# Kernel tuning notes

Measured on AMD Instinct MI355X. Metric: run time of the kernel, lower is better.

## Reference

```python
import jax, jax.numpy as jnp
import numpy as np

NEG_SLOPE = 0.2  # PyG GATConv default leaky_relu slope
N_NODES, N_EDGES, F_IN, HID = 25000, 200000, 64, 128


def gat_layer(x, src, dst, W, a_src, a_dst, b, heads, ch):
    """PyG-style GATConv (concat=True, eval mode). x:[N,Fin] -> [N,heads*ch]."""
    N = x.shape[0]
    h = (x @ W).reshape(N, heads, ch)                      # [N,H,C]
    al_s = jnp.sum(h * a_src, axis=-1)                     # [N,H]
    al_d = jnp.sum(h * a_dst, axis=-1)                     # [N,H]
    e = jax.nn.leaky_relu(al_s[src] + al_d[dst], NEG_SLOPE)  # [E,H]
    # segment softmax over incoming edges of each dst node (stable)
    e = e - jax.ops.segment_max(e, dst, num_segments=N)[dst]
    ex = jnp.exp(e)
    alpha = ex / jax.ops.segment_sum(ex, dst, num_segments=N)[dst]  # [E,H]
    out = jax.ops.segment_sum(h[src] * alpha[:, :, None], dst, num_segments=N)  # [N,H,C]
    return out.reshape(N, heads * ch) + b


def setup_inputs() -> dict:
    key = jax.random.key(0)
    ks = jax.random.split(key, 24)
    def g(k, shape, fan_in):
        return jax.random.normal(k, shape, dtype=jnp.float32) / np.sqrt(fan_in)
    inp = {
        "x": jax.random.normal(ks[0], (N_NODES, F_IN), dtype=jnp.float32),
        "edge_index": jax.random.randint(ks[1], (2, N_EDGES), 0, N_NODES, dtype=jnp.int64) if jax.config.jax_enable_x64 else jax.random.randint(ks[1], (2, N_EDGES), 0, N_NODES).astype(jnp.int32),
        "liquor_idx": jax.random.randint(ks[2], (4096,), 0, N_NODES),
        "ingredient_idx": jax.random.randint(ks[3], (4096,), 0, N_NODES),
        "W1": g(ks[4], (F_IN, 8 * HID), F_IN), "a_s1": g(ks[5], (8, HID), HID), "a_d1": g(ks[6], (8, HID), HID), "b1": jnp.zeros((8 * HID,), jnp.float32),
        "W2": g(ks[7], (8 * HID, 8 * HID), 8 * HID), "a_s2": g(ks[8], (8, HID), HID), "a_d2": g(ks[9], (8, HID), HID), "b2": jnp.zeros((8 * HID,), jnp.float32),
        "W3": g(ks[10], (8 * HID, HID), 8 * HID), "a_s3": g(ks[11], (1, HID), HID), "a_d3": g(ks[12], (1, HID), HID), "b3": jnp.zeros((HID,), jnp.float32),
        # MLP scorer: 256 -> 128 -> 64 -> 1
        "mw1": g(ks[13], (2 * HID, HID), 2 * HID), "mb1": jnp.zeros((HID,), jnp.float32),
        "mw2": g(ks[14], (HID, HID // 2), HID), "mb2": jnp.zeros((HID // 2,), jnp.float32),
        "mw3": g(ks[15], (HID // 2, 1), HID // 2), "mb3": jnp.zeros((1,), jnp.float32),
    }
    return inp


def reference(x, edge_index, liquor_idx, ingredient_idx,
              W1, a_s1, a_d1, b1, W2, a_s2, a_d2, b2, W3, a_s3, a_d3, b3,
              mw1, mb1, mw2, mb2, mw3, mb3):
    N = x.shape[0]
    loops = jnp.arange(N, dtype=edge_index.dtype)  # GATConv adds self-loops
    src = jnp.concatenate([edge_index[0], loops])
    dst = jnp.concatenate([edge_index[1], loops])
    h = jax.nn.relu(gat_layer(x, src, dst, W1, a_s1, a_d1, b1, 8, HID))
    h = jax.nn.relu(gat_layer(h, src, dst, W2, a_s2, a_d2, b2, 8, HID))
    h = gat_layer(h, src, dst, W3, a_s3, a_d3, b3, 1, HID)
    pair = jnp.concatenate([h[liquor_idx], h[ingredient_idx]], axis=-1)  # [B,256]
    z = jax.nn.relu(pair @ mw1 + mb1)
    z = jax.nn.relu(z @ mw2 + mb2)
    z = z @ mw3 + mb3
    return jax.nn.sigmoid(z).squeeze(-1)
```

## Files before the change

kernel.cpp:

```cpp
#include <hip/hip_runtime.h>
#include <math.h>

#define NEG_SLOPE 0.2f

typedef short short8 __attribute__((ext_vector_type(8)));
typedef float f32x4 __attribute__((ext_vector_type(4)));

__device__ __forceinline__ float lrelu(float x){ return x > 0.f ? x : NEG_SLOPE * x; }

__device__ __forceinline__ unsigned short f2bf(float f){
  union { float f; unsigned u; } v; v.f = f;
  unsigned r = v.u + 0x7fff + ((v.u >> 16) & 1);
  return (unsigned short)(r >> 16);
}
__device__ __forceinline__ float bf2f(unsigned short u){
  union { unsigned u; float f; } v; v.u = ((unsigned)u) << 16; return v.f;
}

__device__ __forceinline__ void gld16(const unsigned short* g, unsigned short* l){
  __builtin_amdgcn_global_load_lds(
      (const __attribute__((address_space(1))) unsigned int*)g,
      (__attribute__((address_space(3))) unsigned int*)l, 16, 0, 0);
}

#define MFMA_BF16 __builtin_amdgcn_mfma_f32_16x16x32_bf16

__global__ void k_count(const int* __restrict__ dst, int* __restrict__ cnt, int E){
  int e = blockIdx.x*blockDim.x + threadIdx.x;
  if (e < E) atomicAdd(&cnt[dst[e]], 1);
}

__global__ void k_blockscan(const int* __restrict__ cnt, int* __restrict__ row,
                            int* __restrict__ aux, int n){
  __shared__ int buf[256];
  int t = threadIdx.x;
  int base = blockIdx.x * 256;
  int v = (base + t < n) ? cnt[base + t] : 0;
  buf[t] = v;
  __syncthreads();
  #pragma unroll
  for (int off = 1; off < 256; off <<= 1){
    int u = (t >= off) ? buf[t - off] : 0;
    __syncthreads();
    buf[t] += u;
    __syncthreads();
  }
  if (base + t < n) row[base + t + 1] = buf[t];
  if (t == 255) aux[blockIdx.x] = buf[255];
  if (blockIdx.x == 0 && t == 0) row[0] = 0;
}

__global__ void k_addoff(const int* __restrict__ aux, int* __restrict__ row, int n){
  __shared__ int sbuf[256];
  int b = blockIdx.x, t = threadIdx.x;
  sbuf[t] = (t < b) ? aux[t] : 0;
  __syncthreads();
  #pragma unroll
  for (int off = 128; off >= 1; off >>= 1){
    if (t < off) sbuf[t] += sbuf[t + off];
    __syncthreads();
  }
  int i = b * 256 + t;
  if (i < n) row[i + 1] += sbuf[0];
}

__global__ void k_scatter(const int* __restrict__ src, const int* __restrict__ dst,
                          const int* __restrict__ row, int* __restrict__ cur,
                          int* __restrict__ csr, int E){
  int e = blockIdx.x*blockDim.x + threadIdx.x;
  if (e < E){
    int d = dst[e];
    int p = atomicAdd(&cur[d], 1);
    csr[row[d] + p] = src[e];
  }
}

__global__ void k_prep(const float* __restrict__ x, unsigned short* __restrict__ xb, int nx, int nxb,
                       const float* __restrict__ W1, unsigned short* __restrict__ Wt1,
                       const float* __restrict__ W2, unsigned short* __restrict__ Wt2,
                       const float* __restrict__ W3, unsigned short* __restrict__ Wt3,
                       const float* __restrict__ a_s1, const float* __restrict__ a_d1,
                       float* __restrict__ ws1){
  __shared__ float tile[32][33];
  int b = blockIdx.x, t = threadIdx.x;
  if (b < nxb){
    int i0 = b * 2048 + t * 8;
    if (i0 + 8 <= nx){
      float4 f0 = *reinterpret_cast<const float4*>(x + i0);
      float4 f1 = *reinterpret_cast<const float4*>(x + i0 + 4);
      short8 o;
      o[0]=f2bf(f0.x); o[1]=f2bf(f0.y); o[2]=f2bf(f0.z); o[3]=f2bf(f0.w);
      o[4]=f2bf(f1.x); o[5]=f2bf(f1.y); o[6]=f2bf(f1.z); o[7]=f2bf(f1.w);
      *reinterpret_cast<short8*>(xb + i0) = o;
    } else {
      for (int k = 0; k < 8 && i0 + k < nx; ++k) xb[i0 + k] = f2bf(x[i0 + k]);
    }
    return;
  }
  int bp = b - nxb;
  if (bp >= 64 + 1024 + 128){
    int k = bp - (64 + 1024 + 128);
    int h = t >> 5, lq = t & 31;
    float4 wv = *reinterpret_cast<const float4*>(&W1[(size_t)k * 1024 + h * 128 + lq * 4]);
    float4 sv = *reinterpret_cast<const float4*>(&a_s1[h * 128 + lq * 4]);
    float4 dv = *reinterpret_cast<const float4*>(&a_d1[h * 128 + lq * 4]);
    float ps = wv.x*sv.x + wv.y*sv.y + wv.z*sv.z + wv.w*sv.w;
    float pd = wv.x*dv.x + wv.y*dv.y + wv.z*dv.z + wv.w*dv.w;
    #pragma unroll
    for (int off = 16; off >= 1; off >>= 1){
      ps += __shfl_xor(ps, off);
      pd += __shfl_xor(pd, off);
    }
    if (lq == 0){ ws1[k * 16 + h] = ps; ws1[k * 16 + 8 + h] = pd; }
    return;
  }
  const float* W; unsigned short* Wt; int K, N, ti;
  if (bp < 64)            { W = W1; Wt = Wt1; K = 64;   N = 1024; ti = bp;
                            int kb = (ti & 1) * 32, nb = (ti >> 1) * 32;
                            int tx = t & 31, ty = t >> 5;
                            #pragma unroll
                            for (int i = ty; i < 32; i += 8) tile[i][tx] = W[(size_t)(kb+i)*N + nb+tx];
                            __syncthreads();
                            #pragma unroll
                            for (int i = ty; i < 32; i += 8) Wt[(size_t)(nb+i)*K + kb+tx] = f2bf(tile[tx][i]);
                            return; }
  if (bp < 64 + 1024)     { W = W2; Wt = Wt2; K = 1024; N = 1024; ti = bp - 64; }
  else                    { W = W3; Wt = Wt3; K = 1024; N = 128;  ti = bp - 64 - 1024; }
  int kb = (ti & 31) * 32, nb = (ti >> 5) * 32;
  int tx = t & 31, ty = t >> 5;
  #pragma unroll
  for (int i = ty; i < 32; i += 8) tile[i][tx] = W[(size_t)(kb+i)*N + nb+tx];
  __syncthreads();
  #pragma unroll
  for (int i = ty; i < 32; i += 8) Wt[(size_t)(nb+i)*K + kb+tx] = f2bf(tile[tx][i]);
}

__global__ void k_logits1(const unsigned short* __restrict__ xb, const float* __restrict__ ws,
                          float* __restrict__ ALS, float* __restrict__ ALD, int N){
  __shared__ unsigned short lx[32 * 64];
  __shared__ float lw[64 * 16];
  int t = threadIdx.x;
  int n0 = blockIdx.x * 32;
  int r = t >> 3, c = (t & 7) * 8;
  if (n0 + r < N)
    *reinterpret_cast<short8*>(&lx[r * 64 + c]) =
      *reinterpret_cast<const short8*>(&xb[(size_t)(n0 + r) * 64 + c]);
  else {
    short8 z = {0,0,0,0,0,0,0,0};
    *reinterpret_cast<short8*>(&lx[r * 64 + c]) = z;
  }
  *reinterpret_cast<float4*>(&lw[t * 4]) = *reinterpret_cast<const float4*>(&ws[t * 4]);
  __syncthreads();
  int nl = t >> 3, h = t & 7;
  if (n0 + nl >= N) return;
  float s = 0.f, d = 0.f;
  #pragma unroll 8
  for (int k = 0; k < 64; ++k){
    float xv = bf2f(lx[nl * 64 + k]);
    s = fmaf(xv, lw[k * 16 + h], s);
    d = fmaf(xv, lw[k * 16 + 8 + h], d);
  }
  ALS[(size_t)(n0 + nl) * 8 + h] = s;
  ALD[(size_t)(n0 + nl) * 8 + h] = d;
}

template<int HEADS, int TR>
__global__ void k_sm(const float* __restrict__ ALS, const float* __restrict__ ALD,
                     const int* __restrict__ row, const int* __restrict__ csr,
                     float* __restrict__ alpha, float* __restrict__ alps,
                     float* __restrict__ invl, int N, int E){
  int idx = blockIdx.x * blockDim.x + threadIdx.x;
  int n = idx / HEADS, h = idx - n * HEADS;
  if (n >= N) return;
  float ald = ALD[(size_t)n * HEADS + h];
  float es = lrelu(ALS[(size_t)n * HEADS + h] + ald);
  float m = es;
  int beg = row[n], end = row[n + 1];
  for (int j = beg; j < end; ++j)
    m = fmaxf(m, lrelu(ALS[(size_t)csr[j] * HEADS + h] + ald));
  float ps = __expf(es - m);
  float l = ps;
  for (int j = beg; j < end; ++j){
    float p = __expf(lrelu(ALS[(size_t)csr[j] * HEADS + h] + ald) - m);
    if (TR) alpha[(size_t)h * E + j] = p;
    else    alpha[(size_t)j * HEADS + h] = p;
    l += p;
  }
  alps[(size_t)n * HEADS + h] = ps;
  invl[(size_t)n * HEADS + h] = 1.f / l;
}

__global__ void k_gat_x(const unsigned short* __restrict__ xb, const float* __restrict__ alpha,
                        const float* __restrict__ alps, const float* __restrict__ invl,
                        const int* __restrict__ row, const int* __restrict__ csr,
                        unsigned short* __restrict__ G, int N){
  int t = threadIdx.x;
  int n = blockIdx.x * 4 + (t >> 6);
  if (n >= N) return;
  int lane = t & 63;
  float xv = bf2f(xb[(size_t)n * 64 + lane]);
  float4 s0 = *reinterpret_cast<const float4*>(&alps[(size_t)n * 8]);
  float4 s1 = *reinterpret_cast<const float4*>(&alps[(size_t)n * 8 + 4]);
  float acc[8] = {s0.x*xv, s0.y*xv, s0.z*xv, s0.w*xv, s1.x*xv, s1.y*xv, s1.z*xv, s1.w*xv};
  int beg = row[n], end = row[n + 1];
  for (int j = beg; j < end; ++j){
    int s = csr[j];
    float xs = bf2f(xb[(size_t)s * 64 + lane]);
    float4 a0 = *reinterpret_cast<const float4*>(&alpha[(size_t)j * 8]);
    float4 a1 = *reinterpret_cast<const float4*>(&alpha[(size_t)j * 8 + 4]);
    acc[0] = fmaf(a0.x, xs, acc[0]);
    acc[1] = fmaf(a0.y, xs, acc[1]);
    acc[2] = fmaf(a0.z, xs, acc[2]);
    acc[3] = fmaf(a0.w, xs, acc[3]);
    acc[4] = fmaf(a1.x, xs, acc[4]);
    acc[5] = fmaf(a1.y, xs, acc[5]);
    acc[6] = fmaf(a1.z, xs, acc[6]);
    acc[7] = fmaf(a1.w, xs, acc[7]);
  }
  float4 i0 = *reinterpret_cast<const float4*>(&invl[(size_t)n * 8]);
  float4 i1 = *reinterpret_cast<const float4*>(&invl[(size_t)n * 8 + 4]);
  float iv[8] = {i0.x, i0.y, i0.z, i0.w, i1.x, i1.y, i1.z, i1.w};
  #pragma unroll
  for (int h = 0; h < 8; ++h)
    G[(size_t)n * 512 + h * 64 + lane] = f2bf(acc[h] * iv[h]);
}

__global__ __launch_bounds__(256) void k_gemm_g(
    const unsigned short* __restrict__ G,
    const unsigned short* __restrict__ Bt,
    const float* __restrict__ bias,
    unsigned short* __restrict__ C,
    int M){
  __shared__ unsigned short As[128 * 32];
  __shared__ unsigned short Bs[128 * 32];
  const int nwg = gridDim.x;
  int bid = blockIdx.x;
  int swz = ((nwg & 7) == 0) ? ((bid & 7) * (nwg >> 3) + (bid >> 3)) : bid;
  const int head = swz % 8, byi = swz / 8;
  const int bm = byi * 128, bn = head * 128;
  const int tid  = threadIdx.x;
  const int lane = tid & 63, wave = tid >> 6;
  const int wr = wave >> 1, wc = wave & 1;
  const int lr = lane & 15, lk = lane >> 4;
  const int srow = wave * 16 + (lane >> 2);
  const int skc  = (lane & 3) * 8;
  int ar0 = bm + srow;      if (ar0 >= M) ar0 = M - 1;
  int ar1 = bm + srow + 64; if (ar1 >= M) ar1 = M - 1;
  const unsigned short* ga0 = G + (size_t)ar0 * 512 + head * 64 + skc;
  const unsigned short* ga1 = G + (size_t)ar1 * 512 + head * 64 + skc;
  const unsigned short* gb0 = Bt + (size_t)(bn + srow) * 64 + skc;
  const unsigned short* gb1 = Bt + (size_t)(bn + srow + 64) * 64 + skc;
  f32x4 acc[4][4] = {};
  #pragma unroll
  for (int k0 = 0; k0 < 64; k0 += 32){
    gld16(ga0 + k0, &As[(size_t)wave * 512]);
    gld16(ga1 + k0, &As[(size_t)(wave + 4) * 512]);
    gld16(gb0 + k0, &Bs[(size_t)wave * 512]);
    gld16(gb1 + k0, &Bs[(size_t)(wave + 4) * 512]);
    __syncthreads();
    short8 af[4], bg[4];
    #pragma unroll
    for (int m = 0; m < 4; ++m)
      af[m] = *reinterpret_cast<const short8*>(&As[(wr * 64 + m * 16 + lr) * 32 + lk * 8]);
    #pragma unroll
    for (int n = 0; n < 4; ++n)
      bg[n] = *reinterpret_cast<const short8*>(&Bs[(wc * 64 + n * 16 + lr) * 32 + lk * 8]);
    #pragma unroll
    for (int m = 0; m < 4; ++m)
      #pragma unroll
      for (int n = 0; n < 4; ++n)
        acc[m][n] = MFMA_BF16(af[m], bg[n], acc[m][n], 0, 0, 0);
    __syncthreads();
  }
  float bv[4];
  #pragma unroll
  for (int n = 0; n < 4; ++n) bv[n] = bias[bn + wc * 64 + n * 16 + lr];
  #pragma unroll
  for (int m = 0; m < 4; ++m){
    #pragma unroll
    for (int j = 0; j < 4; ++j){
      int rowi = bm + wr * 64 + m * 16 + lk * 4 + j;
      if (rowi < M){
        #pragma unroll
        for (int n = 0; n < 4; ++n)
          C[(size_t)rowi * 1024 + bn + wc * 64 + n * 16 + lr] = f2bf(fmaxf(acc[m][n][j] + bv[n], 0.f));
      }
    }
  }
}

template<int HEADS>
__global__ __launch_bounds__(256) void k_gemm_fused(
    const unsigned short* __restrict__ A, const unsigned short* __restrict__ Bt,
    unsigned short* __restrict__ C,
    const float* __restrict__ a_s, const float* __restrict__ a_d,
    float* __restrict__ ALS, float* __restrict__ ALD,
    int M, int N, int K, int gxc){
  __shared__ unsigned short SMEM[2 * 128 * 32];
  unsigned short* As = SMEM;
  unsigned short* Bs = SMEM + 128 * 32;
  const int nwg = gridDim.x;
  int bid = blockIdx.x;
  int swz = ((nwg & 7) == 0) ? ((bid & 7) * (nwg >> 3) + (bid >> 3)) : bid;
  const int bxi = swz % gxc, byi = swz / gxc;
  const int bm = byi * 128, bn = bxi * 128;
  const int head = bxi;
  const int tid  = threadIdx.x;
  const int lane = tid & 63, wave = tid >> 6;
  const int wr = wave >> 1, wc = wave & 1;
  const int lr = lane & 15, lk = lane >> 4;
  const int srow = wave * 16 + (lane >> 2);
  const int skc  = (lane & 3) * 8;
  int ar0 = bm + srow;      if (ar0 >= M) ar0 = M - 1;
  int ar1 = bm + srow + 64; if (ar1 >= M) ar1 = M - 1;
  const unsigned short* ga0 = A  + (size_t)ar0 * K + skc;
  const unsigned short* ga1 = A  + (size_t)ar1 * K + skc;
  const unsigned short* gb0 = Bt + (size_t)(bn + srow) * K + skc;
  const unsigned short* gb1 = Bt + (size_t)(bn + srow + 64) * K + skc;
  f32x4 acc[4][4] = {};
  for (int k0 = 0; k0 < K; k0 += 32){
    gld16(ga0 + k0, &As[(size_t)wave * 512]);
    gld16(ga1 + k0, &As[(size_t)(wave + 4) * 512]);
    gld16(gb0 + k0, &Bs[(size_t)wave * 512]);
    gld16(gb1 + k0, &Bs[(size_t)(wave + 4) * 512]);
    __syncthreads();
    short8 af[4], bg[4];
    #pragma unroll
    for (int m = 0; m < 4; ++m)
      af[m] = *reinterpret_cast<const short8*>(&As[(wr * 64 + m * 16 + lr) * 32 + lk * 8]);
    #pragma unroll
    for (int n = 0; n < 4; ++n)
      bg[n] = *reinterpret_cast<const short8*>(&Bs[(wc * 64 + n * 16 + lr) * 32 + lk * 8]);
    #pragma unroll
    for (int m = 0; m < 4; ++m)
      #pragma unroll
      for (int n = 0; n < 4; ++n)
        acc[m][n] = MFMA_BF16(af[m], bg[n], acc[m][n], 0, 0, 0);
    __syncthreads();
  }
  #pragma unroll
  for (int m = 0; m < 4; ++m){
    #pragma unroll
    for (int j = 0; j < 4; ++j){
      int rowi = bm + wr * 64 + m * 16 + lk * 4 + j;
      if (rowi < M){
        #pragma unroll
        for (int n = 0; n < 4; ++n)
          C[(size_t)rowi * N + bn + wc * 64 + n * 16 + lr] = f2bf(acc[m][n][j]);
      }
    }
  }
  float as4[4], ad4[4];
  #pragma unroll
  for (int n = 0; n < 4; ++n){
    as4[n] = a_s[head * 128 + wc * 64 + n * 16 + lr];
    ad4[n] = a_d[head * 128 + wc * 64 + n * 16 + lr];
  }
  float* red = (float*)SMEM;
  #pragma unroll
  for (int m = 0; m < 4; ++m){
    #pragma unroll
    for (int j = 0; j < 4; ++j){
      float ps = 0.f;
      #pragma unroll
      for (int n = 0; n < 4; ++n) ps = fmaf(acc[m][n][j], as4[n], ps);
      red[(wr * 64 + m * 16 + lk * 4 + j) * 32 + wc * 16 + lr] = ps;
    }
  }
  __syncthreads();
  if (tid < 128){
    float s = 0.f;
    #pragma unroll
    for (int i = 0; i < 32; ++i) s += red[tid * 32 + ((i + tid) & 31)];
    int gr = bm + tid;
    if (gr < M) ALS[(size_t)gr * HEADS + head] = s;
  }
  __syncthreads();
  #pragma unroll
  for (int m = 0; m < 4; ++m){
    #pragma unroll
    for (int j = 0; j < 4; ++j){
      float pd = 0.f;
      #pragma unroll
      for (int n = 0; n < 4; ++n) pd = fmaf(acc[m][n][j], ad4[n], pd);
      red[(wr * 64 + m * 16 + lk * 4 + j) * 32 + wc * 16 + lr] = pd;
    }
  }
  __syncthreads();
  if (tid < 128){
    float s = 0.f;
    #pragma unroll
    for (int i = 0; i < 32; ++i) s += red[tid * 32 + ((i + tid) & 31)];
    int gr = bm + tid;
    if (gr < M) ALD[(size_t)gr * HEADS + head] = s;
  }
}

__global__ __launch_bounds__(512, 2) void k_gemm256p8(
    const unsigned short* __restrict__ A,
    const unsigned short* __restrict__ Bt,
    unsigned short* __restrict__ Php,
    const float* __restrict__ a_s, const float* __restrict__ a_d,
    float* __restrict__ ALS, float* __restrict__ ALD,
    int M, int N, int K, int gxc){
  __shared__ unsigned short smem[2 * 32768];
  const int nwg = gridDim.x;
  int bid = blockIdx.x;
  int swz = ((nwg & 7) == 0) ? ((bid & 7) * (nwg >> 3) + (bid >> 3)) : bid;
  const int bxi = swz % gxc, byi = swz / gxc;
  const int bm = byi * 256, bn = bxi * 256;
  const int tid = threadIdx.x;
  const int lane = tid & 63, wave = tid >> 6;
  const int wr = wave >> 2, wc = wave & 3;
  const int lr = lane & 15, lk = lane >> 4;
  const int sr = tid >> 3;
  const int scol = ((tid & 7) << 3) ^ ((sr & 7) << 3);
  unsigned offA[4], offB[4];
  #pragma unroll
  for (int u = 0; u < 4; ++u){
    int r = bm + u * 64 + sr; if (r >= M) r = M - 1;
    offA[u] = (unsigned)r * (unsigned)K + scol;
    offB[u] = (unsigned)(bn + u * 64 + sr) * (unsigned)K + scol;
  }
  const int wdst = wave * 512;
  const int NKT = K >> 6;
  const int NIT = NKT >> 1;

  #define STA(T,u) gld16(A  + (size_t)offA[u] + (size_t)(T)*64, &smem[((T)&1)*32768 + (u)*4096 + wdst])
  #define STB(T,u) gld16(Bt + (size_t)offB[u] + (size_t)(T)*64, &smem[((T)&1)*32768 + 16384 + (u)*4096 + wdst])

  #pragma unroll
  for (int u = 0; u < 4; ++u) STA(0, u);
  #pragma unroll
  for (int u = 0; u < 4; ++u) STB(0, u);
  #pragma unroll
  for (int u = 0; u < 4; ++u) STA(1, u);
  asm volatile("s_waitcnt vmcnt(4)" ::: "memory");
  __builtin_amdgcn_s_barrier();

  f32x4 acc[8][4] = {};
  short8 af[4][2], bg[4][2];

  #define RD_A(moff) \
    _Pragma("unroll") \
    for (int m = 0; m < 4; ++m){ \
      int row = wr * 128 + (m + (moff)) * 16 + lr; \
      int rb = row * 64, sw = (row & 7) << 3; \
      af[m][0] = *reinterpret_cast<const short8*>(&sa[rb + ((lk * 8) ^ sw)]); \
      af[m][1] = *reinterpret_cast<const short8*>(&sa[rb + ((32 + lk * 8) ^ sw)]); \
    }
  #define RD_B(n0_, n1_) \
    _Pragma("unroll") \
    for (int n = (n0_); n < (n1_); ++n){ \
      int row = wc * 64 + n * 16 + lr; \
      int rb = row * 64, sw = (row & 7) << 3; \
      bg[n][0] = *reinterpret_cast<const short8*>(&sb[rb + ((lk * 8) ^ sw)]); \
      bg[n][1] = *reinterpret_cast<const short8*>(&sb[rb + ((32 + lk * 8) ^ sw)]); \
    }
  #define SYNC_MFMA_BEG \
    __builtin_amdgcn_s_barrier(); \
    asm volatile("s_waitcnt lgkmcnt(0)" ::: "memory"); \
    __builtin_amdgcn_sched_barrier(0); \
    __builtin_amdgcn_s_setprio(1);
  #define QUAD(mb, nb) \
    _Pragma("unroll") \
    for (int m = 0; m < 4; ++m) \
      _Pragma("unroll") \
      for (int n = 0; n < 2; ++n){ \
        acc[(mb)+m][(nb)+n] = MFMA_BF16(af[m][0], bg[(nb)+n][0], acc[(mb)+m][(nb)+n], 0, 0, 0); \
        acc[(mb)+m][(nb)+n] = MFMA_BF16(af[m][1], bg[(nb)+n][1], acc[(mb)+m][(nb)+n], 0, 0, 0); \
      }
  #define SYNC_MFMA_END \
    __builtin_amdgcn_s_setprio(0); \
    __builtin_amdgcn_s_barrier();

  for (int it = 0; it < NIT; ++it){
    const int T = it << 1;
    {
      const unsigned short* sa = &smem[(T & 1) * 32768];
      const unsigned short* sb = sa + 16384;
      RD_A(0); RD_B(0, 2);
      STB(T + 1, 0); STB(T + 1, 1);
      SYNC_MFMA_BEG; QUAD(0, 0); SYNC_MFMA_END;
      RD_B(2, 4);
      STB(T + 1, 2); STB(T + 1, 3);
      SYNC_MFMA_BEG; QUAD(0, 2); SYNC_MFMA_END;
      RD_A(4);
      if (T + 2 < NKT){ STA(T + 2, 0); STA(T + 2, 2); }
      SYNC_MFMA_BEG; QUAD(4, 0); SYNC_MFMA_END;
      if (T + 2 < NKT){ STA(T + 2, 1); STA(T + 2, 3); }
      __builtin_amdgcn_s_barrier();
      __builtin_amdgcn_s_setprio(1);
      QUAD(4, 2);
      __builtin_amdgcn_s_setprio(0);
      asm volatile("s_waitcnt vmcnt(4)" ::: "memory");
      __builtin_amdgcn_s_barrier();
    }
    {
      const unsigned short* sa = &smem[((T + 1) & 1) * 32768];
      const unsigned short* sb = sa + 16384;
      RD_A(0); RD_B(0, 2);
      if (T + 2 < NKT){ STB(T + 2, 0); STB(T + 2, 1); }
      SYNC_MFMA_BEG; QUAD(0, 0); SYNC_MFMA_END;
      RD_B(2, 4);
      if (T + 2 < NKT){ STB(T + 2, 2); STB(T + 2, 3); }
      SYNC_MFMA_BEG; QUAD(0, 2); SYNC_MFMA_END;
      RD_A(4);
      if (T + 3 < NKT){ STA(T + 3, 0); STA(T + 3, 2); }
      SYNC_MFMA_BEG; QUAD(4, 0); SYNC_MFMA_END;
      if (T + 3 < NKT){ STA(T + 3, 1); STA(T + 3, 3); }
      __builtin_amdgcn_s_barrier();
      __builtin_amdgcn_s_setprio(1);
      QUAD(4, 2);
      __builtin_amdgcn_s_setprio(0);
      asm volatile("s_waitcnt vmcnt(4)" ::: "memory");
      __builtin_amdgcn_s_barrier();
    }
  }

  const int hloc = wc >> 1;
  const int head = bxi * 2 + hloc;
  const int cc = (wc & 1) * 64;
  #pragma unroll
  for (int m = 0; m < 8; ++m){
    #pragma unroll
    for (int j = 0; j < 4; ++j){
      int row = bm + wr * 128 + m * 16 + lk * 4 + j;
      if (row < M){
        #pragma unroll
        for (int n = 0; n < 4; ++n)
          Php[((size_t)head * M + row) * 128 + cc + n * 16 + lr] = f2bf(acc[m][n][j]);
      }
    }
  }
  float as4[4], ad4[4];
  #pragma unroll
  for (int n = 0; n < 4; ++n){
    as4[n] = a_s[head * 128 + cc + n * 16 + lr];
    ad4[n] = a_d[head * 128 + cc + n * 16 + lr];
  }
  float2* red = (float2*)smem;
  __syncthreads();
  #pragma unroll
  for (int hh = 0; hh < 2; ++hh){
    if (hloc == hh){
      #pragma unroll
      for (int m = 0; m < 8; ++m){
        #pragma unroll
        for (int j = 0; j < 4; ++j){
          float ps = 0.f, pd = 0.f;
          #pragma unroll
          for (int n = 0; n < 4; ++n){
            ps = fmaf(acc[m][n][j], as4[n], ps);
            pd = fmaf(acc[m][n][j], ad4[n], pd);
          }
          red[(wr * 128 + m * 16 + lk * 4 + j) * 32 + (wc & 1) * 16 + lr] = make_float2(ps, pd);
        }
      }
    }
    __syncthreads();
    if (tid < 256){
      float ss = 0.f, sd = 0.f;
      #pragma unroll
      for (int i = 0; i < 32; ++i){
        float2 v = red[tid * 32 + ((i + tid) & 31)];
        ss += v.x; sd += v.y;
      }
      int gr = bm + tid;
      if (gr < M){
        ALS[(size_t)gr * 8 + bxi * 2 + hh] = ss;
        ALD[(size_t)gr * 8 + bxi * 2 + hh] = sd;
      }
    }
    __syncthreads();
  }
  #undef STA
  #undef STB
  #undef RD_A
  #undef RD_B
  #undef SYNC_MFMA_BEG
  #undef QUAD
  #undef SYNC_MFMA_END
}

__global__ void k_gat2h(const unsigned short* __restrict__ Php,
                        const float* __restrict__ alpha,
                        const float* __restrict__ alps, const float* __restrict__ invl,
                        const int* __restrict__ row, const int* __restrict__ csr,
                        const float* __restrict__ bias, unsigned short* __restrict__ outv,
                        int N, int E){
  int h = blockIdx.x & 7;
  int nb = blockIdx.x >> 3;
  int t = threadIdx.x;
  int n = nb * 16 + (t >> 4);
  if (n >= N) return;
  int c0 = (t & 15) * 8;
  const unsigned short* hb = Php + (size_t)h * N * 128;
  const float* alp = alpha + (size_t)h * E;
  float sp = alps[(size_t)n * 8 + h];
  short8 hv8 = *reinterpret_cast<const short8*>(hb + (size_t)n * 128 + c0);
  float accA[8], accB[8] = {};
  #pragma unroll
  for (int v = 0; v < 8; ++v) accA[v] = sp * bf2f((unsigned short)hv8[v]);
  int beg = row[n], end = row[n + 1];
  int j = beg;
  for (; j + 1 < end; j += 2){
    int s0 = csr[j], s1 = csr[j + 1];
    float p0 = alp[j], p1 = alp[j + 1];
    short8 v0 = *reinterpret_cast<const short8*>(hb + (size_t)s0 * 128 + c0);
    short8 v1 = *reinterpret_cast<const short8*>(hb + (size_t)s1 * 128 + c0);
    #pragma unroll
    for (int v = 0; v < 8; ++v){
      accA[v] = fmaf(p0, bf2f((unsigned short)v0[v]), accA[v]);
      accB[v] = fmaf(p1, bf2f((unsigned short)v1[v]), accB[v]);
    }
  }
  if (j < end){
    int s0 = csr[j];
    float p0 = alp[j];
    short8 v0 = *reinterpret_cast<const short8*>(hb + (size_t)s0 * 128 + c0);
    #pragma unroll
    for (int v = 0; v < 8; ++v) accA[v] = fmaf(p0, bf2f((unsigned short)v0[v]), accA[v]);
  }
  float inv = invl[(size_t)n * 8 + h];
  size_t ob = ((size_t)n * 8 + h) * 128 + c0;
  #pragma unroll
  for (int v = 0; v < 8; ++v){
    float o = fmaxf((accA[v] + accB[v]) * inv + bias[h * 128 + c0 + v], 0.f);
    outv[ob + v] = f2bf(o);
  }
}

__global__ void k_pair(const unsigned short* __restrict__ hp,
                       const float* __restrict__ al, const float* __restrict__ aldv,
                       const int* __restrict__ row, const int* __restrict__ csr,
                       const float* __restrict__ bias,
                       const int* __restrict__ liq, const int* __restrict__ ing,
                       const float* __restrict__ mw1, const float* __restrict__ mb1,
                       const float* __restrict__ mw2, const float* __restrict__ mb2,
                       const float* __restrict__ mw3, const float* __restrict__ mb3,
                       float* __restrict__ out, int B){
  __shared__ float pairv[256];
  __shared__ float z1[128];
  __shared__ float z2[64];
  int r = blockIdx.x;
  int t = threadIdx.x;
  int w = t >> 6;
  int lane = t & 63;
  int n = w ? ing[r] : liq[r];
  float ald = aldv[n];
  float es = lrelu(al[n] + ald);
  int beg = row[n], end = row[n + 1];
  float m = es;
  for (int j = beg; j < end; ++j)
    m = fmaxf(m, lrelu(al[csr[j]] + ald));
  float ps = __expf(es - m);
  float l = ps;
  int c0 = lane * 2;
  ushort2 hv = *reinterpret_cast<const ushort2*>(hp + (size_t)n * 128 + c0);
  float a0 = ps * bf2f(hv.x), a1 = ps * bf2f(hv.y);
  for (int j = beg; j < end; ++j){
    int s = csr[j];
    float p = __expf(lrelu(al[s] + ald) - m);
    ushort2 v = *reinterpret_cast<const ushort2*>(hp + (size_t)s * 128 + c0);
    a0 = fmaf(p, bf2f(v.x), a0);
    a1 = fmaf(p, bf2f(v.y), a1);
    l += p;
  }
  float inv = 1.f / l;
  pairv[w * 128 + c0]     = a0 * inv + bias[c0];
  pairv[w * 128 + c0 + 1] = a1 * inv + bias[c0 + 1];
  __syncthreads();
  float acc1 = mb1[t];
  for (int k = 0; k < 256; ++k) acc1 = fmaf(pairv[k], mw1[k * 128 + t], acc1);
  z1[t] = fmaxf(acc1, 0.f);
  __syncthreads();
  if (t < 64){
    float a2 = mb2[t];
    for (int k = 0; k < 128; ++k) a2 = fmaf(z1[k], mw2[k * 64 + t], a2);
    z2[t] = fmaxf(a2, 0.f);
  }
  __syncthreads();
  if (t < 64){
    float p = z2[t] * mw3[t];
    #pragma unroll
    for (int off = 32; off >= 1; off >>= 1) p += __shfl_xor(p, off);
    if (t == 0) out[r] = 1.f / (1.f + __expf(-(p + mb3[0])));
  }
  (void)B;
}

extern "C" void kernel_launch(void* const* d_in, const int* in_sizes, int n_in,
                              void* d_out, int out_size, void* d_ws, size_t ws_size,
                              hipStream_t stream){
  const float* x   = (const float*)d_in[0];
  const int*   ei  = (const int*)  d_in[1];
  const int*   liq = (const int*)  d_in[2];
  const int*   ing = (const int*)  d_in[3];
  const float* W1  = (const float*)d_in[4];
  const float* as1 = (const float*)d_in[5];
  const float* ad1 = (const float*)d_in[6];
  const float* b1  = (const float*)d_in[7];
  const float* W2  = (const float*)d_in[8];
  const float* as2 = (const float*)d_in[9];
  const float* ad2 = (const float*)d_in[10];
  const float* b2  = (const float*)d_in[11];
  const float* W3  = (const float*)d_in[12];
  const float* as3 = (const float*)d_in[13];
  const float* ad3 = (const float*)d_in[14];
  const float* b3  = (const float*)d_in[15];
  const float* mw1 = (const float*)d_in[16];
  const float* mb1 = (const float*)d_in[17];
  const float* mw2 = (const float*)d_in[18];
  const float* mb2 = (const float*)d_in[19];
  const float* mw3 = (const float*)d_in[20];
  const float* mb3 = (const float*)d_in[21];
  float* out = (float*)d_out;

  const int N = in_sizes[0] / 64;
  const int E = in_sizes[1] / 2;
  const int B = in_sizes[2];
  const int* srcp = ei;
  const int* dstp = ei + E;

  char* w = (char*)d_ws;
  auto alloc = [&](size_t bytes) -> char* {
    char* p = w;
    w += (bytes + 255) & ~(size_t)255;
    return p;
  };
  unsigned short* P    = (unsigned short*)alloc((size_t)N * 1024 * 2);
  unsigned short* Hb   = (unsigned short*)alloc((size_t)N * 1024 * 2);
  unsigned short* xb   = (unsigned short*)alloc((size_t)N * 64 * 2);
  unsigned short* Wt1  = (unsigned short*)alloc((size_t)1024 * 64 * 2);
  unsigned short* Wt2  = (unsigned short*)alloc((size_t)1024 * 1024 * 2);
  unsigned short* Wt3  = (unsigned short*)alloc((size_t)128 * 1024 * 2);
  float* ALS  = (float*)alloc((size_t)N * 8 * 4);
  float* ALD  = (float*)alloc((size_t)N * 8 * 4);
  float* alpha= (float*)alloc((size_t)E * 8 * 4);
  float* alps = (float*)alloc((size_t)N * 8 * 4);
  float* invl = (float*)alloc((size_t)N * 8 * 4);
  float* ws1  = (float*)alloc((size_t)64 * 16 * 4);
  int*   row  = (int*)  alloc((size_t)(N + 1) * 4);
  int*   cntcur = (int*)alloc((size_t)2 * N * 4);
  int*   cnt  = cntcur;
  int*   cur  = cntcur + N;
  int*   aux  = (int*)  alloc((size_t)256 * 4);
  int*   csr  = (int*)  alloc((size_t)E * 4);
  unsigned short* G = P;
  (void)ws_size; (void)n_in; (void)out_size;

  int nx = N * 64;
  int nxb = (nx + 2047) / 2048;
  k_prep<<<nxb + 64 + 1024 + 128 + 64, 256, 0, stream>>>(
      x, xb, nx, nxb, W1, Wt1, W2, Wt2, W3, Wt3, as1, ad1, ws1);

  hipMemsetAsync(cntcur, 0, (size_t)2 * N * 4, stream);
  int eb = (E + 255) / 256;
  int nb = (N + 255) / 256;
  k_count<<<eb, 256, 0, stream>>>(dstp, cnt, E);
  k_blockscan<<<nb, 256, 0, stream>>>(cnt, row, aux, N);
  k_addoff<<<nb, 256, 0, stream>>>(aux, row, N);
  k_scatter<<<eb, 256, 0, stream>>>(srcp, dstp, row, cur, csr, E);

  const int mt  = (N + 127) / 128;
  const int mt2 = (N + 255) / 256;
  const int smb8 = (N * 8 + 255) / 256;

  k_logits1<<<(N + 31) / 32, 256, 0, stream>>>(xb, ws1, ALS, ALD, N);
  k_sm<8,0><<<smb8, 256, 0, stream>>>(ALS, ALD, row, csr, alpha, alps, invl, N, E);
  k_gat_x<<<(N + 3) / 4, 256, 0, stream>>>(xb, alpha, alps, invl, row, csr, G, N);
  k_gemm_g<<<8 * mt, 256, 0, stream>>>(G, Wt1, b1, Hb, N);

  k_gemm256p8<<<4 * mt2, 512, 0, stream>>>(Hb, Wt2, P, as2, ad2, ALS, ALD, N, 1024, 1024, 4);
  k_sm<8,1><<<smb8, 256, 0, stream>>>(ALS, ALD, row, csr, alpha, alps, invl, N, E);
  k_gat2h<<<8 * ((N + 15) / 16), 256, 0, stream>>>(P, alpha, alps, invl, row, csr, b2, Hb, N, E);

  k_gemm_fused<1><<<1 * mt, 256, 0, stream>>>(Hb, Wt3, P, as3, ad3, ALS, ALD, N, 128, 1024, 1);
  k_pair<<<B, 128, 0, stream>>>(P, ALS, ALD, row, csr, b3, liq, ing,
                                mw1, mb1, mw2, mb2, mw3, mb3, out, B);
}
```

Baseline: 305.1 us.

## Restructure GEMM main loop to load full K-tile fragments up front with fewer barriers

```diff
diff --git a/kernel.cpp b/kernel.cpp
--- a/kernel.cpp
+++ b/kernel.cpp
@@ -424,7 +424,6 @@
   }
   const int wdst = wave * 512;
   const int NKT = K >> 6;
-  const int NIT = NKT >> 1;
 
   #define STA(T,u) gld16(A  + (size_t)offA[u] + (size_t)(T)*64, &smem[((T)&1)*32768 + (u)*4096 + wdst])
   #define STB(T,u) gld16(Bt + (size_t)offB[u] + (size_t)(T)*64, &smem[((T)&1)*32768 + 16384 + (u)*4096 + wdst])
@@ -439,83 +438,61 @@
   __builtin_amdgcn_s_barrier();
 
   f32x4 acc[8][4] = {};
-  short8 af[4][2], bg[4][2];
-
-  #define RD_A(moff) \
+  short8 afA[4][2], afB[4][2], bg[4][2];
+
+  #define RD_AF(dst, moff) \
     _Pragma("unroll") \
     for (int m = 0; m < 4; ++m){ \
       int row = wr * 128 + (m + (moff)) * 16 + lr; \
       int rb = row * 64, sw = (row & 7) << 3; \
-      af[m][0] = *reinterpret_cast<const short8*>(&sa[rb + ((lk * 8) ^ sw)]); \
-      af[m][1] = *reinterpret_cast<const short8*>(&sa[rb + ((32 + lk * 8) ^ sw)]); \
-    }
-  #define RD_B(n0_, n1_) \
+      dst[m][0] = *reinterpret_cast<const short8*>(&sa[rb + ((lk * 8) ^ sw)]); \
+      dst[m][1] = *reinterpret_cast<const short8*>(&sa[rb + ((32 + lk * 8) ^ sw)]); \
+    }
+  #define RD_BG() \
     _Pragma("unroll") \
-    for (int n = (n0_); n < (n1_); ++n){ \
+    for (int n = 0; n < 4; ++n){ \
       int row = wc * 64 + n * 16 + lr; \
       int rb = row * 64, sw = (row & 7) << 3; \
       bg[n][0] = *reinterpret_cast<const short8*>(&sb[rb + ((lk * 8) ^ sw)]); \
       bg[n][1] = *reinterpret_cast<const short8*>(&sb[rb + ((32 + lk * 8) ^ sw)]); \
     }
-  #define SYNC_MFMA_BEG \
-    __builtin_amdgcn_s_barrier(); \
-    asm volatile("s_waitcnt lgkmcnt(0)" ::: "memory"); \
-    __builtin_amdgcn_sched_barrier(0); \
-    __builtin_amdgcn_s_setprio(1);
-  #define QUAD(mb, nb) \
+  #define QUADX(src, mb, nb) \
     _Pragma("unroll") \
     for (int m = 0; m < 4; ++m) \
       _Pragma("unroll") \
       for (int n = 0; n < 2; ++n){ \
-        acc[(mb)+m][(nb)+n] = MFMA_BF16(af[m][0], bg[(nb)+n][0], acc[(mb)+m][(nb)+n], 0, 0, 0); \
-        acc[(mb)+m][(nb)+n] = MFMA_BF16(af[m][1], bg[(nb)+n][1], acc[(mb)+m][(nb)+n], 0, 0, 0); \
+        acc[(mb)+m][(nb)+n] = MFMA_BF16(src[m][0], bg[(nb)+n][0], acc[(mb)+m][(nb)+n], 0, 0, 0); \
+        acc[(mb)+m][(nb)+n] = MFMA_BF16(src[m][1], bg[(nb)+n][1], acc[(mb)+m][(nb)+n], 0, 0, 0); \
       }
-  #define SYNC_MFMA_END \
-    __builtin_amdgcn_s_setprio(0); \
+
+  for (int kt = 0; kt < NKT; ++kt){
+    const unsigned short* sa = &smem[(kt & 1) * 32768];
+    const unsigned short* sb = sa + 16384;
+    RD_AF(afA, 0);
+    RD_AF(afB, 4);
+    RD_BG();
+    if (kt + 1 < NKT){ STB(kt + 1, 0); STB(kt + 1, 1); }
     __builtin_amdgcn_s_barrier();
-
-  for (int it = 0; it < NIT; ++it){
-    const int T = it << 1;
-    {
-      const unsigned short* sa = &smem[(T & 1) * 32768];
-      const unsigned short* sb = sa + 16384;
-      RD_A(0); RD_B(0, 2);
-      STB(T + 1, 0); STB(T + 1, 1);
-      SYNC_MFMA_BEG; QUAD(0, 0); SYNC_MFMA_END;
-      RD_B(2, 4);
-      STB(T + 1, 2); STB(T + 1, 3);
-      SYNC_MFMA_BEG; QUAD(0, 2); SYNC_MFMA_END;
-      RD_A(4);
-      if (T + 2 < NKT){ STA(T + 2, 0); STA(T + 2, 2); }
-      SYNC_MFMA_BEG; QUAD(4, 0); SYNC_MFMA_END;
-      if (T + 2 < NKT){ STA(T + 2, 1); STA(T + 2, 3); }
-      __builtin_amdgcn_s_barrier();
-      __builtin_amdgcn_s_setprio(1);
-      QUAD(4, 2);
-      __builtin_amdgcn_s_setprio(0);
-      asm volatile("s_waitcnt vmcnt(4)" ::: "memory");
-      __builtin_amdgcn_s_barrier();
-    }
-    {
-      const unsigned short* sa = &smem[((T + 1) & 1) * 32768];
-      const unsigned short* sb = sa + 16384;
-      RD_A(0); RD_B(0, 2);
-      if (T + 2 < NKT){ STB(T + 2, 0); STB(T + 2, 1); }
-      SYNC_MFMA_BEG; QUAD(0, 0); SYNC_MFMA_END;
-      RD_B(2, 4);
-      if (T + 2 < NKT){ STB(T + 2, 2); STB(T + 2, 3); }
-      SYNC_MFMA_BEG; QUAD(0, 2); SYNC_MFMA_END;
-      RD_A(4);
-      if (T + 3 < NKT){ STA(T + 3, 0); STA(T + 3, 2); }
-      SYNC_MFMA_BEG; QUAD(4, 0); SYNC_MFMA_END;
-      if (T + 3 < NKT){ STA(T + 3, 1); STA(T + 3, 3); }
-      __builtin_amdgcn_s_barrier();
-      __builtin_amdgcn_s_setprio(1);
-      QUAD(4, 2);
-      __builtin_amdgcn_s_setprio(0);
-      asm volatile("s_waitcnt vmcnt(4)" ::: "memory");
-      __builtin_amdgcn_s_barrier();
-    }
+    asm volatile("s_waitcnt lgkmcnt(0)" ::: "memory");
+    __builtin_amdgcn_sched_barrier(0);
+    __builtin_amdgcn_s_setprio(1);
+    QUADX(afA, 0, 0);
+    __builtin_amdgcn_s_setprio(0);
+    __builtin_amdgcn_s_barrier();
+    if (kt + 1 < NKT){ STB(kt + 1, 2); STB(kt + 1, 3); }
+    __builtin_amdgcn_s_setprio(1);
+    QUADX(afA, 0, 2);
+    __builtin_amdgcn_s_setprio(0);
+    if (kt + 2 < NKT){ STA(kt + 2, 0); STA(kt + 2, 2); }
+    __builtin_amdgcn_s_setprio(1);
+    QUADX(afB, 4, 0);
+    __builtin_amdgcn_s_setprio(0);
+    if (kt + 2 < NKT){ STA(kt + 2, 1); STA(kt + 2, 3); }
+    __builtin_amdgcn_s_setprio(1);
+    QUADX(afB, 4, 2);
+    __builtin_amdgcn_s_setprio(0);
+    asm volatile("s_waitcnt vmcnt(4)" ::: "memory");
+    __builtin_amdgcn_s_barrier();
   }
 
   const int hloc = wc >> 1;
@@ -539,6 +516,8 @@
     as4[n] = a_s[head * 128 + cc + n * 16 + lr];
     ad4[n] = a_d[head * 128 + cc + n * 16 + lr];
   }
+  asm volatile("s_waitcnt vmcnt(0)" ::: "memory");
+  __builtin_amdgcn_s_barrier();
   float2* red = (float2*)smem;
   __syncthreads();
   #pragma unroll
@@ -576,11 +555,9 @@
   }
   #undef STA
   #undef STB
-  #undef RD_A
-  #undef RD_B
-  #undef SYNC_MFMA_BEG
-  #undef QUAD
-  #undef SYNC_MFMA_END
+  #undef RD_AF
+  #undef RD_BG
+  #undef QUADX
 }
 
 __global__ void k_gat2h(const unsigned short* __restrict__ Php,
```

Result: no change. 305.8 us (+0.2%).
